# Optimization experiments

Hardware: AMD Instinct MI355X
Metric: run time of the kernel (lower is better)

## Reference

```python
import jax, jax.numpy as jnp
import numpy as np

B, S, D, H = 4, 2048, 1024, 16
HD = D // H

def setup_inputs() -> dict:
    key = jax.random.key(0)
    ks = jax.random.split(key, 5)
    scale = 1.0 / np.sqrt(D)
    x = jax.random.normal(ks[0], (B, S, D), dtype=jnp.float32)
    w_qkv = jax.random.normal(ks[1], (D, 3 * D), dtype=jnp.float32) * scale
    b_qkv = jax.random.normal(ks[2], (3 * D,), dtype=jnp.float32) * 0.01
    w_proj = jax.random.normal(ks[3], (D, D), dtype=jnp.float32) * scale
    b_proj = jax.random.normal(ks[4], (D,), dtype=jnp.float32) * 0.01
    return {"x": x, "w_qkv": w_qkv, "b_qkv": b_qkv, "w_proj": w_proj, "b_proj": b_proj}

def reference(x, w_qkv, b_qkv, w_proj, b_proj):
    b, s, d = x.shape
    qkv = x @ w_qkv + b_qkv                      # [B,S,3D]
    qkv = qkv.reshape(b, s, 3, H, HD)
    q, k, v = jnp.moveaxis(qkv, 2, 0)            # each [B,S,H,HD]
    q = q.transpose(0, 2, 1, 3)                  # [B,H,S,HD]
    k = k.transpose(0, 2, 1, 3)
    v = v.transpose(0, 2, 1, 3)
    scale = 1.0 / jnp.sqrt(jnp.asarray(HD, dtype=x.dtype))
    scores = jnp.einsum('bhqd,bhkd->bhqk', q, k) * scale
    attn = jax.nn.softmax(scores, axis=-1)
    out = jnp.einsum('bhqk,bhkd->bhqd', attn, v)  # [B,H,S,HD]
    out = out.transpose(0, 2, 1, 3).reshape(b, s, d)
    return out @ w_proj + b_proj
```

## Files before the change

### kernel.cpp

```cpp
#include <hip/hip_runtime.h>

#define B_  4
#define S_  2048
#define D_  1024
#define H_  16
#define HD_ 64
#define M_  (B_*S_)
#define QSCALE 0.1803368801111204f

typedef unsigned short u16;
typedef __bf16 bf16x8 __attribute__((ext_vector_type(8)));
typedef __bf16 bf16x2 __attribute__((ext_vector_type(2)));
typedef float  f32x4  __attribute__((ext_vector_type(4)));
typedef float  f32x16 __attribute__((ext_vector_type(16)));

__device__ __forceinline__ u16 f2bf(float f) {
  unsigned int u = __float_as_uint(f);
  u += 0x7fffu + ((u >> 16) & 1u);
  return (u16)(u >> 16);
}
__device__ __forceinline__ unsigned int packbf2(float lo, float hi) {
#if __has_builtin(__builtin_amdgcn_cvt_pk_bf16_f32)
  union { bf16x2 v; unsigned int u; } c;
  c.v = __builtin_amdgcn_cvt_pk_bf16_f32(lo, hi);
  return c.u;
#else
  return (unsigned int)f2bf(lo) | ((unsigned int)f2bf(hi) << 16);
#endif
}
__device__ __forceinline__ void gld16(const void* g, void* l) {
  __builtin_amdgcn_global_load_lds(
      (const __attribute__((address_space(1))) unsigned int*)g,
      (__attribute__((address_space(3))) unsigned int*)l, 16, 0, 0);
}
#define WAIT_VM8() asm volatile("s_waitcnt vmcnt(8)" ::: "memory")
#define WAIT_VM0() asm volatile("s_waitcnt vmcnt(0)" ::: "memory")
#define MFMA32(a,b,c) __builtin_amdgcn_mfma_f32_32x32x16_bf16(a,b,c,0,0,0)
#define MFMA16(a,b,c) __builtin_amdgcn_mfma_f32_16x16x32_bf16(a,b,c,0,0,0)

__device__ __forceinline__ size_t off16e(int r, int k) {
  return ((size_t)((r >> 7) * 32 + (k >> 5))) * 4096
       + (size_t)((r >> 4) & 7) * 512
       + (size_t)(((k >> 3) & 3) * 16 + (r & 15)) * 8 + (k & 7);
}
__device__ __forceinline__ size_t offA32(int bh, int s, int hd) {
  return ((size_t)(bh * 32 + (s >> 6)) * 8 + ((s >> 5) & 1) * 4 + (hd >> 4)) * 512
       + (size_t)(((hd >> 3) & 1) * 32 + (s & 31)) * 8 + (hd & 7);
}
__device__ __forceinline__ size_t offVT(int bh, int s, int hd) {
  return ((size_t)(bh * 32 + (s >> 6)) * 8 + (hd >> 5) * 4 + ((s >> 4) & 3)) * 512
       + (size_t)(((s >> 3) & 1) * 32 + (hd & 31)) * 8 + (s & 7);
}

__global__ void cvt_f32_bf16(const float* __restrict__ in, u16* __restrict__ out, int n4) {
  int i = blockIdx.x * 256 + threadIdx.x;
  if (i < n4) {
    float4 v = ((const float4*)in)[i];
    int m = i >> 8;
    int k = (i & 255) * 4;
    *(uint2*)&out[off16e(m, k)] = make_uint2(packbf2(v.x, v.y), packbf2(v.z, v.w));
  }
}

__global__ void transpose_w(const float* __restrict__ in, u16* __restrict__ out, int R, int C) {
  __shared__ float tile[32][33];
  int c0 = blockIdx.x * 32, r0 = blockIdx.y * 32;
  int tx = threadIdx.x, ty = threadIdx.y;
  #pragma unroll
  for (int i = 0; i < 4; i++)
    tile[ty + i*8][tx] = in[(size_t)(r0 + ty + i*8) * C + c0 + tx];
  __syncthreads();
  #pragma unroll
  for (int i = 0; i < 4; i++)
    out[off16e(c0 + ty + i*8, r0 + tx)] = f2bf(tile[tx][ty + i*8]);
}

__global__ __launch_bounds__(256,2) void gemm_qkv(
    const u16* __restrict__ X, const u16* __restrict__ WT,
    const float* __restrict__ bias,
    u16* __restrict__ qb, u16* __restrict__ kb, u16* __restrict__ vb)
{
  __shared__ u16 As[2*8*512];
  __shared__ u16 Bs[2*8*512];
  const int t = threadIdx.x, w = t >> 6, l = t & 63;
  const int m0 = blockIdx.y * 128, n0 = blockIdx.x * 128;
  const u16* Ab = X  + (size_t)(m0 >> 7) * 32 * 4096;
  const u16* Bb = WT + (size_t)(n0 >> 7) * 32 * 4096;

  #pragma unroll
  for (int f2 = 0; f2 < 2; f2++) {
    gld16(Ab + (w*2+f2)*512 + l*8, (char*)As + (w*2+f2)*1024);
    gld16(Bb + (w*2+f2)*512 + l*8, (char*)Bs + (w*2+f2)*1024);
  }
  f32x4 acc[4][4] = {};
  const int af = (w >> 1) * 4, bf = (w & 1) * 4;
  for (int it = 0; it < 32; it++) {
    __syncthreads();
    const int cur = (it & 1) * 4096;
    if (it < 31) {
      const int nb = ((it + 1) & 1) * 8;
      const size_t gs = (size_t)(it + 1) * 4096;
      #pragma unroll
      for (int f2 = 0; f2 < 2; f2++) {
        gld16(Ab + gs + (w*2+f2)*512 + l*8, (char*)As + (nb + w*2+f2)*1024);
        gld16(Bb + gs + (w*2+f2)*512 + l*8, (char*)Bs + (nb + w*2+f2)*1024);
      }
    }
    bf16x8 a[4], b[4];
    #pragma unroll
    for (int mt = 0; mt < 4; mt++) a[mt] = *(const bf16x8*)(As + cur + (af+mt)*512 + l*8);
    #pragma unroll
    for (int nt = 0; nt < 4; nt++) b[nt] = *(const bf16x8*)(Bs + cur + (bf+nt)*512 + l*8);
    #pragma unroll
    for (int mt = 0; mt < 4; mt++)
      #pragma unroll
      for (int nt = 0; nt < 4; nt++)
        acc[mt][nt] = MFMA16(a[mt], b[nt], acc[mt][nt]);
  }
  const int wm = (w >> 1) * 64, wn = (w & 1) * 64, lr = l & 15, quad = l >> 4;
  #pragma unroll
  for (int mt = 0; mt < 4; mt++)
  #pragma unroll
  for (int nt = 0; nt < 4; nt++) {
    int n = n0 + wn + nt * 16 + lr;
    float bia = bias[n];
    int which = n >> 10, hh = (n >> 6) & 15, hd = n & 63;
    #pragma unroll
    for (int r = 0; r < 4; r++) {
      int m = m0 + wm + mt * 16 + quad * 4 + r;
      float v = acc[mt][nt][r] + bia;
      int bb = m >> 11, s = m & 2047, bh = bb * 16 + hh;
      if (which == 0)      qb[offA32(bh, s, hd)] = f2bf(v * QSCALE);
      else if (which == 1) kb[offA32(bh, s, hd)] = f2bf(v);
      else                 vb[offVT(bh, s, hd)] = f2bf(v);
    }
  }
}

__global__ __launch_bounds__(256,2) void gemm_proj(
    const u16* __restrict__ X, const u16* __restrict__ WT,
    const float* __restrict__ bias, float* __restrict__ out)
{
  __shared__ u16 As[2*8*512];
  __shared__ u16 Bs[2*8*512];
  const int t = threadIdx.x, w = t >> 6, l = t & 63;
  const int m0 = blockIdx.y * 128, n0 = blockIdx.x * 128;
  const u16* Ab = X  + (size_t)(m0 >> 7) * 32 * 4096;
  const u16* Bb = WT + (size_t)(n0 >> 7) * 32 * 4096;

  #pragma unroll
  for (int f2 = 0; f2 < 2; f2++) {
    gld16(Ab + (w*2+f2)*512 + l*8, (char*)As + (w*2+f2)*1024);
    gld16(Bb + (w*2+f2)*512 + l*8, (char*)Bs + (w*2+f2)*1024);
  }
  f32x4 acc[4][4] = {};
  const int af = (w >> 1) * 4, bf = (w & 1) * 4;
  for (int it = 0; it < 32; it++) {
    __syncthreads();
    const int cur = (it & 1) * 4096;
    if (it < 31) {
      const int nb = ((it + 1) & 1) * 8;
      const size_t gs = (size_t)(it + 1) * 4096;
      #pragma unroll
      for (int f2 = 0; f2 < 2; f2++) {
        gld16(Ab + gs + (w*2+f2)*512 + l*8, (char*)As + (nb + w*2+f2)*1024);
        gld16(Bb + gs + (w*2+f2)*512 + l*8, (char*)Bs + (nb + w*2+f2)*1024);
      }
    }
    bf16x8 a[4], b[4];
    #pragma unroll
    for (int mt = 0; mt < 4; mt++) a[mt] = *(const bf16x8*)(As + cur + (af+mt)*512 + l*8);
    #pragma unroll
    for (int nt = 0; nt < 4; nt++) b[nt] = *(const bf16x8*)(Bs + cur + (bf+nt)*512 + l*8);
    #pragma unroll
    for (int mt = 0; mt < 4; mt++)
      #pragma unroll
      for (int nt = 0; nt < 4; nt++)
        acc[mt][nt] = MFMA16(a[mt], b[nt], acc[mt][nt]);
  }
  const int wm = (w >> 1) * 64, wn = (w & 1) * 64, lr = l & 15, quad = l >> 4;
  #pragma unroll
  for (int mt = 0; mt < 4; mt++)
  #pragma unroll
  for (int nt = 0; nt < 4; nt++) {
    int n = n0 + wn + nt * 16 + lr;
    float bia = bias[n];
    #pragma unroll
    for (int r = 0; r < 4; r++) {
      int m = m0 + wm + mt * 16 + quad * 4 + r;
      out[(size_t)m * D_ + n] = acc[mt][nt][r] + bia;
    }
  }
}

__global__ __launch_bounds__(256,4) void attn(
    const u16* __restrict__ qb, const u16* __restrict__ kb,
    const u16* __restrict__ vt, u16* __restrict__ ob)
{
  __shared__ u16 Ks[2][8*512];
  __shared__ u16 Vs[2][8*512];
  __shared__ float redL[4][32];
  const int t = threadIdx.x, w = t >> 6, l = t & 63, l31 = l & 31, h = l >> 5;
  const int i = blockIdx.x, xcd = i & 7, j = i >> 3;
  const int bh = xcd * 8 + (j >> 4), qt = j & 15;
  const int b = bh >> 4, hh = bh & 15;
  const int s0 = qt * 128 + w * 32;
  const u16* qp = qb + (size_t)bh * 131072;
  const u16* kp = kb + (size_t)bh * 131072;
  const u16* vp = vt + (size_t)bh * 131072;

  bf16x8 qa[4];
  {
    const size_t qbase = ((size_t)(qt*2 + (w >> 1)) * 8 + (w & 1) * 4) * 512;
    #pragma unroll
    for (int kk = 0; kk < 4; kk++)
      qa[kk] = *(const bf16x8*)(qp + qbase + (size_t)kk * 512 + l*8);
  }

  f32x16 o[2] = {};
  float l_ = 0.f;

  #pragma unroll
  for (int c = 0; c < 2; c++) {
    gld16(kp + (size_t)(w*2 + c) * 512 + l*8, (char*)&Ks[0][0] + (w*2 + c)*1024);
    gld16(vp + (size_t)(w*2 + c) * 512 + l*8, (char*)&Vs[0][0] + (w*2 + c)*1024);
  }
  WAIT_VM0();
  __syncthreads();

  for (int kt = 0; kt < 32; kt++) {
    const int cur = kt & 1, nxt = cur ^ 1;
    const u16* Kb = &Ks[cur][0];
    const u16* Vb = &Vs[cur][0];

    if (kt < 31) {
      const size_t gs = (size_t)(kt + 1) * 4096;
      #pragma unroll
      for (int c = 0; c < 2; c++) {
        gld16(kp + gs + (size_t)(w*2 + c) * 512 + l*8, (char*)&Ks[nxt][0] + (w*2 + c)*1024);
        gld16(vp + gs + (size_t)(w*2 + c) * 512 + l*8, (char*)&Vs[nxt][0] + (w*2 + c)*1024);
      }
    }

    f32x16 sf[2] = {};
    #pragma unroll
    for (int kk = 0; kk < 4; kk++) {
      bf16x8 ka0 = *(const bf16x8*)(Kb + (0*4 + kk)*512 + l*8);
      bf16x8 ka1 = *(const bf16x8*)(Kb + (1*4 + kk)*512 + l*8);
      sf[0] = MFMA32(ka0, qa[kk], sf[0]);
      sf[1] = MFMA32(ka1, qa[kk], sf[1]);
    }

    unsigned int pk[2][4][2];
    {
      float sa = 0.f, sb = 0.f, sc = 0.f, sd = 0.f;
      #pragma unroll
      for (int mt = 0; mt < 2; mt++)
        #pragma unroll
        for (int e = 0; e < 4; e++) {
          float p0 = __builtin_amdgcn_exp2f(sf[mt][4*e+0]);
          float p1 = __builtin_amdgcn_exp2f(sf[mt][4*e+1]);
          float p2 = __builtin_amdgcn_exp2f(sf[mt][4*e+2]);
          float p3 = __builtin_amdgcn_exp2f(sf[mt][4*e+3]);
          sa += p0; sb += p1; sc += p2; sd += p3;
          pk[mt][e][0] = packbf2(p0, p1);
          pk[mt][e][1] = packbf2(p2, p3);
        }
      float s = (sa + sb) + (sc + sd);
      s += __shfl_xor(s, 32);
      l_ += s;
    }

    #pragma unroll
    for (int kk2 = 0; kk2 < 4; kk2++) {
      const int mt = kk2 >> 1, k1 = kk2 & 1;
      bf16x8 bv0 = *(const bf16x8*)(Vb + (0*4 + kk2)*512 + l*8);
      bf16x8 bv1 = *(const bf16x8*)(Vb + (1*4 + kk2)*512 + l*8);
      unsigned int s0_ = h ? pk[mt][2*k1][0] : pk[mt][2*k1+1][0];
      unsigned int s1_ = h ? pk[mt][2*k1][1] : pk[mt][2*k1+1][1];
      unsigned int r0 = (unsigned int)__shfl_xor((int)s0_, 32);
      unsigned int r1 = (unsigned int)__shfl_xor((int)s1_, 32);
      union { unsigned int u[4]; bf16x8 v; } pa;
      pa.u[0] = h ? r0 : pk[mt][2*k1][0];
      pa.u[1] = h ? r1 : pk[mt][2*k1][1];
      pa.u[2] = h ? pk[mt][2*k1+1][0] : r0;
      pa.u[3] = h ? pk[mt][2*k1+1][1] : r1;
      o[0] = MFMA32(pa.v, bv0, o[0]);
      o[1] = MFMA32(pa.v, bv1, o[1]);
    }

    if (kt < 31) {
      WAIT_VM0();
      __syncthreads();
    }
  }

  redL[w][l31] = 1.f / l_;
  __syncthreads();
  #pragma unroll
  for (int rb = 0; rb < 4; rb++) {
    f32x4 iv4 = *(const f32x4*)&redL[w][8*rb + 4*h];
    #pragma unroll
    for (int c = 0; c < 4; c++) {
      int r = rb*4 + c;
      int row = s0 + c + 8*rb + 4*h;
      int m = b * S_ + row;
      int d0 = hh*64 + l31, d1 = hh*64 + 32 + l31;
      ob[off16e(m, d0)] = f2bf(o[0][r] * iv4[c]);
      ob[off16e(m, d1)] = f2bf(o[1][r] * iv4[c]);
    }
  }
}

extern "C" void kernel_launch(void* const* d_in, const int* in_sizes, int n_in,
                              void* d_out, int out_size, void* d_ws, size_t ws_size,
                              hipStream_t stream) {
  const float* x      = (const float*)d_in[0];
  const float* w_qkv  = (const float*)d_in[1];
  const float* b_qkv  = (const float*)d_in[2];
  const float* w_proj = (const float*)d_in[3];
  const float* b_proj = (const float*)d_in[4];
  float* out = (float*)d_out;

  char* ws = (char*)d_ws;
  u16* xbf    = (u16*)ws; ws += (size_t)M_ * D_ * 2;
  u16* wqkvT  = (u16*)ws; ws += (size_t)3 * D_ * D_ * 2;
  u16* wprojT = (u16*)ws; ws += (size_t)D_ * D_ * 2;
  u16* qbuf   = (u16*)ws; ws += (size_t)M_ * D_ * 2;
  u16* kbuf   = (u16*)ws; ws += (size_t)M_ * D_ * 2;
  u16* vtbuf  = (u16*)ws; ws += (size_t)M_ * D_ * 2;
  u16* aobuf  = (u16*)ws; ws += (size_t)M_ * D_ * 2;

  cvt_f32_bf16<<<(M_ * D_ / 4 + 255) / 256, 256, 0, stream>>>(x, xbf, M_ * D_ / 4);
  transpose_w<<<dim3(3 * D_ / 32, D_ / 32), dim3(32, 8), 0, stream>>>(w_qkv, wqkvT, D_, 3 * D_);
  transpose_w<<<dim3(D_ / 32, D_ / 32), dim3(32, 8), 0, stream>>>(w_proj, wprojT, D_, D_);
  gemm_qkv<<<dim3(3 * D_ / 128, M_ / 128), 256, 0, stream>>>(xbf, wqkvT, b_qkv, qbuf, kbuf, vtbuf);
  attn<<<1024, 256, 0, stream>>>(qbuf, kbuf, vtbuf, aobuf);
  gemm_proj<<<dim3(D_ / 128, M_ / 128), 256, 0, stream>>>(aobuf, wprojT, b_proj, out);
}
```

Baseline: 318.9 us.

## Widen GEMM tiles to 128x256 with 8 waves and finer-grained pipelined mainloop

Both GEMMs now share one mainloop that uses 512-thread blocks computing 128x256 output tiles. Each iteration covers two 32-wide K sub-tiles, interleaving async global-to-LDS prefetch with MFMA work. Raw s_barrier, vmcnt waits and s_setprio keep the matrix units fed. The wider N tile raises A-tile reuse and halves the grid, at the cost of more LDS per block and fewer blocks to fill the CUs.

```diff
diff --git a/kernel.cpp b/kernel.cpp
--- a/kernel.cpp
+++ b/kernel.cpp
@@ -33,7 +33,7 @@
       (const __attribute__((address_space(1))) unsigned int*)g,
       (__attribute__((address_space(3))) unsigned int*)l, 16, 0, 0);
 }
-#define WAIT_VM8() asm volatile("s_waitcnt vmcnt(8)" ::: "memory")
+#define WAIT_VM3() asm volatile("s_waitcnt vmcnt(3)" ::: "memory")
 #define WAIT_VM0() asm volatile("s_waitcnt vmcnt(0)" ::: "memory")
 #define MFMA32(a,b,c) __builtin_amdgcn_mfma_f32_32x32x16_bf16(a,b,c,0,0,0)
 #define MFMA16(a,b,c) __builtin_amdgcn_mfma_f32_16x16x32_bf16(a,b,c,0,0,0)
@@ -75,49 +75,79 @@
     out[off16e(c0 + ty + i*8, r0 + tx)] = f2bf(tile[tx][ty + i*8]);
 }
 
-__global__ __launch_bounds__(256,2) void gemm_qkv(
+__device__ __forceinline__ void gemm_mainloop(
+    const u16* __restrict__ Ab, const u16* __restrict__ Bb0,
+    const u16* __restrict__ Bb1, u16* As, u16* Bs,
+    f32x4 (&acc)[4][4], const int t, const int w, const int l)
+{
+  const int wm4 = (w >> 2) * 4;
+  const int ct  = (w & 3) >> 1;
+  const int wn1 = w & 1;
+
+  #pragma unroll
+  for (int kg = 0; kg < 2; ++kg) {
+    gld16(Ab  + (size_t)kg * 4096 + t*8, (char*)(As + (0*2 + kg)*4096) + w*1024);
+    gld16(Bb0 + (size_t)kg * 4096 + t*8, (char*)(Bs + ((0*2 + 0)*2 + kg)*4096) + w*1024);
+    gld16(Bb1 + (size_t)kg * 4096 + t*8, (char*)(Bs + ((0*2 + 1)*2 + kg)*4096) + w*1024);
+  }
+  WAIT_VM0();
+  __syncthreads();
+
+  for (int kt = 0; kt < 16; ++kt) {
+    const int cur = kt & 1, nxt = cur ^ 1;
+    #pragma unroll
+    for (int kk = 0; kk < 2; ++kk) {
+      bf16x8 a[4], b[4];
+      const u16* Ar = As + (cur*2 + kk)*4096;
+      const u16* Br = Bs + ((cur*2 + ct)*2 + kk)*4096;
+      #pragma unroll
+      for (int mt = 0; mt < 4; ++mt)
+        a[mt] = *(const bf16x8*)(Ar + (wm4 + mt)*512 + l*8);
+      #pragma unroll
+      for (int nt = 0; nt < 4; ++nt)
+        b[nt] = *(const bf16x8*)(Br + (wn1*4 + nt)*512 + l*8);
+
+      if (kt < 15) {
+        const size_t gs = (size_t)((kt + 1)*2 + kk) * 4096 + t*8;
+        gld16(Ab  + gs, (char*)(As + (nxt*2 + kk)*4096) + w*1024);
+        gld16(Bb0 + gs, (char*)(Bs + ((nxt*2 + 0)*2 + kk)*4096) + w*1024);
+        gld16(Bb1 + gs, (char*)(Bs + ((nxt*2 + 1)*2 + kk)*4096) + w*1024);
+      }
+
+      __builtin_amdgcn_s_barrier();
+      asm volatile("s_waitcnt lgkmcnt(0)" ::: "memory");
+      __builtin_amdgcn_s_setprio(1);
+      #pragma unroll
+      for (int mt = 0; mt < 4; ++mt)
+        #pragma unroll
+        for (int nt = 0; nt < 4; ++nt)
+          acc[mt][nt] = MFMA16(a[mt], b[nt], acc[mt][nt]);
+      __builtin_amdgcn_s_setprio(0);
+
+      if (kt < 15)      { WAIT_VM3(); }
+      else if (kk == 0) { WAIT_VM0(); }
+      __builtin_amdgcn_s_barrier();
+    }
+  }
+}
+
+__global__ __launch_bounds__(512,2) void gemm_qkv(
     const u16* __restrict__ X, const u16* __restrict__ WT,
     const float* __restrict__ bias,
     u16* __restrict__ qb, u16* __restrict__ kb, u16* __restrict__ vb)
 {
-  __shared__ u16 As[2*8*512];
-  __shared__ u16 Bs[2*8*512];
+  __shared__ u16 As[2*2*4096];
+  __shared__ u16 Bs[2*2*2*4096];
   const int t = threadIdx.x, w = t >> 6, l = t & 63;
-  const int m0 = blockIdx.y * 128, n0 = blockIdx.x * 128;
-  const u16* Ab = X  + (size_t)(m0 >> 7) * 32 * 4096;
-  const u16* Bb = WT + (size_t)(n0 >> 7) * 32 * 4096;
-
-  #pragma unroll
-  for (int f2 = 0; f2 < 2; f2++) {
-    gld16(Ab + (w*2+f2)*512 + l*8, (char*)As + (w*2+f2)*1024);
-    gld16(Bb + (w*2+f2)*512 + l*8, (char*)Bs + (w*2+f2)*1024);
-  }
+  const int m0 = blockIdx.y * 128, n0 = blockIdx.x * 256;
+  const u16* Ab  = X  + (size_t)blockIdx.y * 32 * 4096;
+  const u16* Bb0 = WT + (size_t)(2*blockIdx.x + 0) * 32 * 4096;
+  const u16* Bb1 = WT + (size_t)(2*blockIdx.x + 1) * 32 * 4096;
+
   f32x4 acc[4][4] = {};
-  const int af = (w >> 1) * 4, bf = (w & 1) * 4;
-  for (int it = 0; it < 32; it++) {
-    __syncthreads();
-    const int cur = (it & 1) * 4096;
-    if (it < 31) {
-      const int nb = ((it + 1) & 1) * 8;
-      const size_t gs = (size_t)(it + 1) * 4096;
-      #pragma unroll
-      for (int f2 = 0; f2 < 2; f2++) {
-        gld16(Ab + gs + (w*2+f2)*512 + l*8, (char*)As + (nb + w*2+f2)*1024);
-        gld16(Bb + gs + (w*2+f2)*512 + l*8, (char*)Bs + (nb + w*2+f2)*1024);
-      }
-    }
-    bf16x8 a[4], b[4];
-    #pragma unroll
-    for (int mt = 0; mt < 4; mt++) a[mt] = *(const bf16x8*)(As + cur + (af+mt)*512 + l*8);
-    #pragma unroll
-    for (int nt = 0; nt < 4; nt++) b[nt] = *(const bf16x8*)(Bs + cur + (bf+nt)*512 + l*8);
-    #pragma unroll
-    for (int mt = 0; mt < 4; mt++)
-      #pragma unroll
-      for (int nt = 0; nt < 4; nt++)
-        acc[mt][nt] = MFMA16(a[mt], b[nt], acc[mt][nt]);
-  }
-  const int wm = (w >> 1) * 64, wn = (w & 1) * 64, lr = l & 15, quad = l >> 4;
+  gemm_mainloop(Ab, Bb0, Bb1, As, Bs, acc, t, w, l);
+
+  const int wm = (w >> 2) * 64, wn = (w & 3) * 64, lr = l & 15, quad = l >> 4;
   #pragma unroll
   for (int mt = 0; mt < 4; mt++)
   #pragma unroll
@@ -137,48 +167,22 @@
   }
 }
 
-__global__ __launch_bounds__(256,2) void gemm_proj(
+__global__ __launch_bounds__(512,2) void gemm_proj(
     const u16* __restrict__ X, const u16* __restrict__ WT,
     const float* __restrict__ bias, float* __restrict__ out)
 {
-  __shared__ u16 As[2*8*512];
-  __shared__ u16 Bs[2*8*512];
+  __shared__ u16 As[2*2*4096];
+  __shared__ u16 Bs[2*2*2*4096];
   const int t = threadIdx.x, w = t >> 6, l = t & 63;
-  const int m0 = blockIdx.y * 128, n0 = blockIdx.x * 128;
-  const u16* Ab = X  + (size_t)(m0 >> 7) * 32 * 4096;
-  const u16* Bb = WT + (size_t)(n0 >> 7) * 32 * 4096;
-
-  #pragma unroll
-  for (int f2 = 0; f2 < 2; f2++) {
-    gld16(Ab + (w*2+f2)*512 + l*8, (char*)As + (w*2+f2)*1024);
-    gld16(Bb + (w*2+f2)*512 + l*8, (char*)Bs + (w*2+f2)*1024);
-  }
+  const int m0 = blockIdx.y * 128, n0 = blockIdx.x * 256;
+  const u16* Ab  = X  + (size_t)blockIdx.y * 32 * 4096;
+  const u16* Bb0 = WT + (size_t)(2*blockIdx.x + 0) * 32 * 4096;
+  const u16* Bb1 = WT + (size_t)(2*blockIdx.x + 1) * 32 * 4096;
+
   f32x4 acc[4][4] = {};
-  const int af = (w >> 1) * 4, bf = (w & 1) * 4;
-  for (int it = 0; it < 32; it++) {
-    __syncthreads();
-    const int cur = (it & 1) * 4096;
-    if (it < 31) {
-      const int nb = ((it + 1) & 1) * 8;
-      const size_t gs = (size_t)(it + 1) * 4096;
-      #pragma unroll
-      for (int f2 = 0; f2 < 2; f2++) {
-        gld16(Ab + gs + (w*2+f2)*512 + l*8, (char*)As + (nb + w*2+f2)*1024);
-        gld16(Bb + gs + (w*2+f2)*512 + l*8, (char*)Bs + (nb + w*2+f2)*1024);
-      }
-    }
-    bf16x8 a[4], b[4];
-    #pragma unroll
-    for (int mt = 0; mt < 4; mt++) a[mt] = *(const bf16x8*)(As + cur + (af+mt)*512 + l*8);
-    #pragma unroll
-    for (int nt = 0; nt < 4; nt++) b[nt] = *(const bf16x8*)(Bs + cur + (bf+nt)*512 + l*8);
-    #pragma unroll
-    for (int mt = 0; mt < 4; mt++)
-      #pragma unroll
-      for (int nt = 0; nt < 4; nt++)
-        acc[mt][nt] = MFMA16(a[mt], b[nt], acc[mt][nt]);
-  }
-  const int wm = (w >> 1) * 64, wn = (w & 1) * 64, lr = l & 15, quad = l >> 4;
+  gemm_mainloop(Ab, Bb0, Bb1, As, Bs, acc, t, w, l);
+
+  const int wm = (w >> 2) * 64, wn = (w & 3) * 64, lr = l & 15, quad = l >> 4;
   #pragma unroll
   for (int mt = 0; mt < 4; mt++)
   #pragma unroll
@@ -334,7 +338,7 @@
   cvt_f32_bf16<<<(M_ * D_ / 4 + 255) / 256, 256, 0, stream>>>(x, xbf, M_ * D_ / 4);
   transpose_w<<<dim3(3 * D_ / 32, D_ / 32), dim3(32, 8), 0, stream>>>(w_qkv, wqkvT, D_, 3 * D_);
   transpose_w<<<dim3(D_ / 32, D_ / 32), dim3(32, 8), 0, stream>>>(w_proj, wprojT, D_, D_);
-  gemm_qkv<<<dim3(3 * D_ / 128, M_ / 128), 256, 0, stream>>>(xbf, wqkvT, b_qkv, qbuf, kbuf, vtbuf);
+  gemm_qkv<<<dim3(3 * D_ / 256, M_ / 128), 512, 0, stream>>>(xbf, wqkvT, b_qkv, qbuf, kbuf, vtbuf);
   attn<<<1024, 256, 0, stream>>>(qbuf, kbuf, vtbuf, aobuf);
-  gemm_proj<<<dim3(D_ / 128, M_ / 128), 256, 0, stream>>>(aobuf, wprojT, b_proj, out);
-}
+  gemm_proj<<<dim3(D_ / 256, M_ / 128), 512, 0, stream>>>(aobuf, wprojT, b_proj, out);
+}
```

Result: faster. 305.0 us (-4.4%).
